# Kernel tuning notes

Hardware: AMD Instinct MI355X
Metric: run time of the kernel (lower is better)

Reference implementation:

```python
import jax, jax.numpy as jnp
import numpy as np

HID = 256
N, D, K, EPOCHS = 100000, 512, 5, 2


def _lin(x, w, b):
    return x @ w.T + b


def setup_inputs() -> dict:
    key = jax.random.key(0)
    ks = jax.random.split(key, 16)
    s = 0.05
    return {
        "x0": jax.random.normal(ks[0], (N, D), jnp.float32),
        "x1": jax.random.normal(ks[1], (N, D), jnp.float32),
        "Hin0_w": jax.random.normal(ks[2], (HID, D), jnp.float32) * s,
        "Hin0_b": jax.random.normal(ks[3], (HID,), jnp.float32) * s,
        "Hin1_w": jax.random.normal(ks[4], (HID, D), jnp.float32) * s,
        "Hin1_b": jax.random.normal(ks[5], (HID,), jnp.float32) * s,
        "w0_w": jax.random.normal(ks[6], (HID, HID), jnp.float32) * s,
        "w0_b": jax.random.normal(ks[7], (HID,), jnp.float32) * s,
        "w1_w": jax.random.normal(ks[8], (HID, HID), jnp.float32) * s,
        "w1_b": jax.random.normal(ks[9], (HID,), jnp.float32) * s,
        "w2_w": jax.random.normal(ks[10], (HID, HID), jnp.float32) * s,
        "w2_b": jax.random.normal(ks[11], (HID,), jnp.float32) * s,
        "edge0": jax.random.randint(ks[12], (2, N * K), 0, N, dtype=jnp.int32),
        "edge1": jax.random.randint(ks[13], (2, N * K), 0, N, dtype=jnp.int32),
        "k": K,
        "update_epoch": EPOCHS,
    }


def reference(x0, x1, Hin0_w, Hin0_b, Hin1_w, Hin1_b, w0_w, w0_b,
              w1_w, w1_b, w2_w, w2_b, edge0, edge1, k, update_epoch):
    xs = (x0, x1)
    edges = (edge0, edge1)
    Hws = ((Hin0_w, Hin0_b), (Hin1_w, Hin1_b))
    n_views = len(xs)

    # per-view input projections: h_init[v] = H_ins[v](train_view[v])
    h_inits = [_lin(x, w, b) for x, (w, b) in zip(xs, Hws)]

    finals = []
    for v in range(n_views):
        # neighbor table: node i's k neighbors are edge[1][i*k : (i+1)*k]
        nbr_idx = edges[v][1].reshape(-1, k)  # [N, k]
        # cross-view self term: mean over other views of w2(h_init_other)
        slf = _lin(h_inits[1 - v], w2_w, w2_b)  # [N, HID] (nv-1 == 1)
        h = h_inits[v]
        for _ in range(update_epoch):
            h = _lin(h, w0_w, w0_b)
            # mean_j w1(h[nbr_j]) == w1(mean_j h[nbr_j]) since w1 is affine
            nbr_mean = h[nbr_idx].mean(axis=1)  # [N, HID] gather + reduce
            h = h + _lin(nbr_mean, w1_w, w1_b) + slf
        finals.append(jax.nn.relu(h))

    # average final embeddings across views
    h_out = sum(finals) / n_views
    return h_out
```

## Files before the change

### kernel.cpp

```cpp
#include <hip/hip_runtime.h>

#define NN 100000
#define DD 512
#define HH 256
#define KNB 5

typedef __attribute__((ext_vector_type(8))) short short8v;
typedef __attribute__((ext_vector_type(4))) short short4v;
typedef __attribute__((ext_vector_type(4))) float float4v;

static __device__ __forceinline__ float bf2f(unsigned short u) {
  union { unsigned int i; float f; } c;
  c.i = ((unsigned int)u) << 16;
  return c.f;
}
static __device__ __forceinline__ unsigned short f2bf(float f) {
  union { float f; unsigned int i; } c;
  c.f = f;
  unsigned int u = c.i;
  u += 0x7FFFu + ((u >> 16) & 1u);
  return (unsigned short)(u >> 16);
}

#define GLOAD16(g, l) __builtin_amdgcn_global_load_lds( \
    (const __attribute__((address_space(1))) unsigned int*)(g), \
    (__attribute__((address_space(3))) unsigned int*)(l), 16, 0, 0)

__global__ void cvt2(const float* __restrict__ s0, short* __restrict__ d0,
                     const float* __restrict__ s1, short* __restrict__ d1) {
  const int S1 = (HH * DD) / 4;
  int i = blockIdx.x * blockDim.x + threadIdx.x;
  if (i >= 2 * S1) return;
  const float* s = (i < S1) ? s0 : s1;
  short* d = (i < S1) ? d0 : d1;
  int j = (i < S1) ? i : i - S1;
  float4 v = reinterpret_cast<const float4*>(s)[j];
  short4v o;
  o[0] = (short)f2bf(v.x); o[1] = (short)f2bf(v.y);
  o[2] = (short)f2bf(v.z); o[3] = (short)f2bf(v.w);
  reinterpret_cast<short4v*>(d)[j] = o;
}

__global__ void prep_w01(const float* __restrict__ w0, const float* __restrict__ w1,
                         const float* __restrict__ w2, const float* __restrict__ b0,
                         const float* __restrict__ b1, const float* __restrict__ b2,
                         short* __restrict__ Bcat, float* __restrict__ bc) {
  int i = blockIdx.x;
  int j = threadIdx.x;
  Bcat[(size_t)i * 768 + j]       = (short)f2bf(w0[i * 256 + j]);
  Bcat[(size_t)i * 768 + 512 + j] = (short)f2bf(w2[i * 256 + j]);
  float acc = 0.f;
  for (int k = 0; k < 256; ++k)
    acc = fmaf(w1[i * 256 + k], w0[k * 256 + j], acc);
  Bcat[(size_t)i * 768 + 256 + j] = (short)f2bf(acc);
  if (j == 0) {
    float s = b0[i] + b1[i] + b2[i];
    for (int k = 0; k < 256; ++k) s = fmaf(w1[i * 256 + k], b0[k], s);
    bc[i] = s;
  }
}

__global__ __launch_bounds__(512, 2) void proj_k(
    const float* __restrict__ Af0, const float* __restrict__ Af1,
    const short* __restrict__ Bw0, const short* __restrict__ Bw1,
    const float* __restrict__ bi0, const float* __restrict__ bi1,
    short* __restrict__ Cb0, short* __restrict__ Cb1)
{
  const float* Af = blockIdx.y ? Af1 : Af0;
  const short* Bw = blockIdx.y ? Bw1 : Bw0;
  const float* bias = blockIdx.y ? bi1 : bi0;
  short* Cb = blockIdx.y ? Cb1 : Cb0;

  __shared__ __align__(16) char BsRaw[2 * 256 * 64 * 2];
  __shared__ __align__(16) char AsRaw[2 * 64 * 64 * 2];

  const int tid = threadIdx.x;
  const int lane = tid & 63;
  const int wave = tid >> 6;
  const int wr = wave >> 2;
  const int wc = wave & 3;
  const int row0 = blockIdx.x * 64;

  const int sr = tid >> 3;
  const int slc = (tid & 7) ^ (sr & 7);
  const int srg = min(row0 + sr, NN - 1);
  const float* Asrc = Af + (size_t)srg * DD + slc * 8;

  int brow[4], blc[4];
#pragma unroll
  for (int q = 0; q < 4; ++q) {
    int ch = q * 512 + tid;
    brow[q] = ch >> 3;
    blc[q] = (ch & 7) ^ (brow[q] & 7);
  }

  float4v acc[2][4];
#pragma unroll
  for (int m = 0; m < 2; ++m)
#pragma unroll
    for (int n = 0; n < 4; ++n) acc[m][n] = (float4v)0.f;

  float4 pa[2][2];
  short8v pb[4];

#pragma unroll
  for (int q = 0; q < 4; ++q)
    pb[q] = *reinterpret_cast<const short8v*>(Bw + (size_t)brow[q] * DD + blc[q] * 8);
  {
    float4 f0 = *reinterpret_cast<const float4*>(Asrc);
    float4 f1 = *reinterpret_cast<const float4*>(Asrc + 4);
    short8v o;
    o[0] = (short)f2bf(f0.x); o[1] = (short)f2bf(f0.y);
    o[2] = (short)f2bf(f0.z); o[3] = (short)f2bf(f0.w);
    o[4] = (short)f2bf(f1.x); o[5] = (short)f2bf(f1.y);
    o[6] = (short)f2bf(f1.z); o[7] = (short)f2bf(f1.w);
    *reinterpret_cast<short8v*>(AsRaw + tid * 16) = o;
  }
#pragma unroll
  for (int q = 0; q < 4; ++q)
    *reinterpret_cast<short8v*>(BsRaw + (q * 512 + tid) * 16) = pb[q];
  pa[1][0] = *reinterpret_cast<const float4*>(Asrc + 64);
  pa[1][1] = *reinterpret_cast<const float4*>(Asrc + 68);
  __syncthreads();

#pragma unroll
  for (int s = 0; s < 8; ++s) {
    if (s + 1 < 8) {
#pragma unroll
      for (int q = 0; q < 4; ++q)
        pb[q] = *reinterpret_cast<const short8v*>(
            Bw + (size_t)brow[q] * DD + (s + 1) * 64 + blc[q] * 8);
    }
    if (s + 2 < 8) {
      pa[s & 1][0] = *reinterpret_cast<const float4*>(Asrc + (s + 2) * 64);
      pa[s & 1][1] = *reinterpret_cast<const float4*>(Asrc + (s + 2) * 64 + 4);
    }
    {
      const char* Bc = BsRaw + (s & 1) * 32768;
      const char* Ac = AsRaw + (s & 1) * 8192;
#pragma unroll
      for (int kk = 0; kk < 2; ++kk) {
        const int ckb = kk * 4 + (lane >> 4);
        short8v a[2], b[4];
#pragma unroll
        for (int n = 0; n < 4; ++n) {
          int rb = wc * 64 + n * 16 + (lane & 15);
          b[n] = *reinterpret_cast<const short8v*>(Bc + rb * 128 + ((ckb ^ (rb & 7)) << 4));
        }
#pragma unroll
        for (int m = 0; m < 2; ++m) {
          int ra = wr * 32 + m * 16 + (lane & 15);
          a[m] = *reinterpret_cast<const short8v*>(Ac + ra * 128 + ((ckb ^ (ra & 7)) << 4));
        }
#pragma unroll
        for (int m = 0; m < 2; ++m)
#pragma unroll
          for (int n = 0; n < 4; ++n)
            acc[m][n] = __builtin_amdgcn_mfma_f32_16x16x32_bf16(b[n], a[m], acc[m][n], 0, 0, 0);
      }
    }
    if (s + 1 < 8) {
      char* Bn = BsRaw + ((s + 1) & 1) * 32768;
#pragma unroll
      for (int q = 0; q < 4; ++q)
        *reinterpret_cast<short8v*>(Bn + (q * 512 + tid) * 16) = pb[q];
      float4 f0 = pa[(s + 1) & 1][0];
      float4 f1 = pa[(s + 1) & 1][1];
      short8v o;
      o[0] = (short)f2bf(f0.x); o[1] = (short)f2bf(f0.y);
      o[2] = (short)f2bf(f0.z); o[3] = (short)f2bf(f0.w);
      o[4] = (short)f2bf(f1.x); o[5] = (short)f2bf(f1.y);
      o[6] = (short)f2bf(f1.z); o[7] = (short)f2bf(f1.w);
      *reinterpret_cast<short8v*>(AsRaw + ((s + 1) & 1) * 8192 + tid * 16) = o;
    }
    __syncthreads();
  }

  const int crow = lane & 15;
  const int cg = (lane >> 4) * 4;
#pragma unroll
  for (int m = 0; m < 2; ++m) {
    int rg = row0 + wr * 32 + m * 16 + crow;
    if (rg >= NN) continue;
#pragma unroll
    for (int n = 0; n < 4; ++n) {
      int colb = wc * 64 + n * 16 + cg;
      size_t off = (size_t)rg * HH + colb;
      float4v bi = *reinterpret_cast<const float4v*>(bias + colb);
      short4v o;
#pragma unroll
      for (int i = 0; i < 4; ++i) o[i] = (short)f2bf(acc[m][n][i] + bi[i]);
      *reinterpret_cast<short4v*>(Cb + off) = o;
    }
  }
}

template<int EPI>
__global__ __launch_bounds__(512, 4) void epoch_k(
    const short* __restrict__ D, const short* __restrict__ Cc,
    const short* __restrict__ Bw, const float* __restrict__ bias,
    short* __restrict__ Ob, float* __restrict__ Of,
    const short* __restrict__ Fin, const int* __restrict__ nbr)
{
  __shared__ __align__(16) char BsRaw[256 * 64 * 2];
  __shared__ __align__(16) char AsRaw[128 * 64 * 2];
  __shared__ int nbrL[128][KNB];

  const int tid = threadIdx.x;
  const int lane = tid & 63;
  const int wave = tid >> 6;
  const int wr = wave >> 2;
  const int wc = wave & 3;
  const int row0 = blockIdx.x * 128;

  for (int e = tid; e < 128 * KNB; e += 512) {
    int r = e / KNB;
    int rg = min(row0 + r, NN - 1);
    nbrL[r][e - r * KNB] = nbr[rg * KNB + (e - r * KNB)];
  }

  float4v acc[4][4];
#pragma unroll
  for (int m = 0; m < 4; ++m)
#pragma unroll
    for (int n = 0; n < 4; ++n) acc[m][n] = (float4v)0.f;

  for (int k0 = 0; k0 < 768; k0 += 64) {
#pragma unroll
    for (int q = 0; q < 4; ++q) {
      int ch = q * 512 + tid;
      int r = ch >> 3, pc = ch & 7;
      int lc = pc ^ (r & 7);
      GLOAD16(Bw + (size_t)r * 768 + k0 + lc * 8, BsRaw + (q * 512 + wave * 64) * 16);
    }
    if (k0 < 256 || k0 >= 512) {
      const short* H = (k0 < 256) ? (D + k0) : (Cc + (k0 - 512));
#pragma unroll
      for (int q = 0; q < 2; ++q) {
        int ch = q * 512 + tid;
        int r = ch >> 3, pc = ch & 7;
        int lc = pc ^ (r & 7);
        int rg = min(row0 + r, NN - 1);
        GLOAD16(H + (size_t)rg * HH + lc * 8, AsRaw + (q * 512 + wave * 64) * 16);
      }
    } else {
      const int kb = k0 - 256;
#pragma unroll
      for (int q = 0; q < 2; ++q) {
        int ch = q * 512 + tid;
        int r = ch >> 3, pc = ch & 7;
        int lc = pc ^ (r & 7);
        float a8[8] = {0.f, 0.f, 0.f, 0.f, 0.f, 0.f, 0.f, 0.f};
#pragma unroll
        for (int j = 0; j < KNB; ++j) {
          int id = nbrL[r][j];
          short8v v = *reinterpret_cast<const short8v*>(D + (size_t)id * HH + kb + lc * 8);
#pragma unroll
          for (int x = 0; x < 8; ++x) a8[x] += bf2f((unsigned short)v[x]);
        }
        short8v o;
#pragma unroll
        for (int x = 0; x < 8; ++x) o[x] = (short)f2bf(a8[x] * 0.2f);
        *reinterpret_cast<short8v*>(AsRaw + ch * 16) = o;
      }
    }
    __syncthreads();

#pragma unroll
    for (int kk = 0; kk < 2; ++kk) {
      const int ckb = kk * 4 + (lane >> 4);
      short8v a[4], b[4];
#pragma unroll
      for (int n = 0; n < 4; ++n) {
        int rb = wc * 64 + n * 16 + (lane & 15);
        b[n] = *reinterpret_cast<const short8v*>(BsRaw + rb * 128 + ((ckb ^ (rb & 7)) << 4));
      }
#pragma unroll
      for (int m = 0; m < 4; ++m) {
        int ra = wr * 64 + m * 16 + (lane & 15);
        a[m] = *reinterpret_cast<const short8v*>(AsRaw + ra * 128 + ((ckb ^ (ra & 7)) << 4));
      }
#pragma unroll
      for (int m = 0; m < 4; ++m)
#pragma unroll
        for (int n = 0; n < 4; ++n)
          acc[m][n] = __builtin_amdgcn_mfma_f32_16x16x32_bf16(b[n], a[m], acc[m][n], 0, 0, 0);
    }
    __syncthreads();
  }

  const int crow = lane & 15;
  const int cg = (lane >> 4) * 4;
#pragma unroll
  for (int m = 0; m < 4; ++m) {
    int rg = row0 + wr * 64 + m * 16 + crow;
    if (rg >= NN) continue;
#pragma unroll
    for (int n = 0; n < 4; ++n) {
      int colb = wc * 64 + n * 16 + cg;
      size_t off = (size_t)rg * HH + colb;
      float4v bi = *reinterpret_cast<const float4v*>(bias + colb);
      float v[4];
#pragma unroll
      for (int i = 0; i < 4; ++i) v[i] = acc[m][n][i] + bi[i];
      if constexpr (EPI >= 2) {
#pragma unroll
        for (int i = 0; i < 4; ++i) v[i] = fmaxf(v[i], 0.f);
      }
      if constexpr (EPI <= 2) {
        short4v o;
#pragma unroll
        for (int i = 0; i < 4; ++i) o[i] = (short)f2bf(v[i]);
        *reinterpret_cast<short4v*>(Ob + off) = o;
      } else {
        short4v f4 = *reinterpret_cast<const short4v*>(Fin + off);
        float4v o;
#pragma unroll
        for (int i = 0; i < 4; ++i)
          o[i] = (v[i] + bf2f((unsigned short)f4[i])) * 0.5f;
        *reinterpret_cast<float4v*>(Of + off) = o;
      }
    }
  }
}

extern "C" void kernel_launch(void* const* d_in, const int* in_sizes, int n_in,
                              void* d_out, int out_size, void* d_ws, size_t ws_size,
                              hipStream_t stream) {
  const float* x0  = (const float*)d_in[0];
  const float* x1  = (const float*)d_in[1];
  const float* wh0 = (const float*)d_in[2];
  const float* bh0 = (const float*)d_in[3];
  const float* wh1 = (const float*)d_in[4];
  const float* bh1 = (const float*)d_in[5];
  const float* w0  = (const float*)d_in[6];
  const float* b0  = (const float*)d_in[7];
  const float* w1  = (const float*)d_in[8];
  const float* b1  = (const float*)d_in[9];
  const float* w2  = (const float*)d_in[10];
  const float* b2  = (const float*)d_in[11];
  const int* e0    = (const int*)d_in[12];
  const int* e1    = (const int*)d_in[13];
  const int* nbr0  = e0 + (size_t)NN * KNB;
  const int* nbr1  = e1 + (size_t)NN * KNB;
  float* out       = (float*)d_out;

  char* ws = (char*)d_ws;
  size_t off = 0;
  auto alloc = [&](size_t bytes) -> void* {
    off = (off + 255) & ~(size_t)255;
    void* p = ws + off;
    off += bytes;
    return p;
  };

  short* Wh0  = (short*)alloc((size_t)HH * DD * 2);
  short* Wh1  = (short*)alloc((size_t)HH * DD * 2);
  short* Bcat = (short*)alloc((size_t)HH * 768 * 2);
  float* bc   = (float*)alloc((size_t)HH * 4);
  const size_t NB = (size_t)NN * HH * 2;
  short* hi0 = (short*)alloc(NB);
  short* hi1 = (short*)alloc(NB);
  short* hb0 = (short*)alloc(NB);
  short* hb1 = (short*)alloc(NB);
  short* f0  = (short*)alloc(NB);

  cvt2<<<dim3(256), dim3(256), 0, stream>>>(wh0, Wh0, wh1, Wh1);
  prep_w01<<<dim3(256), dim3(256), 0, stream>>>(w0, w1, w2, b0, b1, b2, Bcat, bc);

  proj_k<<<dim3((NN + 63) / 64, 2), dim3(512), 0, stream>>>(
      x0, x1, Wh0, Wh1, bh0, bh1, hi0, hi1);

  dim3 ge((NN + 127) / 128);

  epoch_k<0><<<ge, dim3(512), 0, stream>>>(hi0, hi1, Bcat, bc, hb0, nullptr, nullptr, nbr0);
  epoch_k<0><<<ge, dim3(512), 0, stream>>>(hi1, hi0, Bcat, bc, hb1, nullptr, nullptr, nbr1);

  epoch_k<2><<<ge, dim3(512), 0, stream>>>(hb0, hi1, Bcat, bc, f0, nullptr, nullptr, nbr0);
  epoch_k<3><<<ge, dim3(512), 0, stream>>>(hb1, hi0, Bcat, bc, nullptr, out, f0, nbr1);

  (void)in_sizes; (void)n_in; (void)out_size; (void)ws_size;
}
```

Measured before the change: 532.6 us.

## Double-buffer epoch GEMM stages and merge first-epoch views into one launch

Rewrites the epoch kernel's K loop as an explicitly unrolled, double-buffered pipeline. The next stage's async global-to-LDS loads are issued while the current stage's MFMAs run, using manual vmcnt waits and raw barriers in place of __syncthreads. The two first-epoch launches are merged into one launch with a 2D grid that picks the view from blockIdx.y. The aim is to hide load latency and cut launch overhead and tail effects, at the cost of doubled LDS use (about 96KB), which lowers occupancy, and the launch-bounds occupancy hint is dropped.

```diff
diff --git a/kernel.cpp b/kernel.cpp
--- a/kernel.cpp
+++ b/kernel.cpp
@@ -25,6 +25,10 @@
 #define GLOAD16(g, l) __builtin_amdgcn_global_load_lds( \
     (const __attribute__((address_space(1))) unsigned int*)(g), \
     (__attribute__((address_space(3))) unsigned int*)(l), 16, 0, 0)
+
+#define WAITV(N) asm volatile("s_waitcnt vmcnt(" #N ")" ::: "memory")
+#define WAITL()  asm volatile("s_waitcnt lgkmcnt(0)" ::: "memory")
+#define BAR()    __builtin_amdgcn_s_barrier()
 
 __global__ void cvt2(const float* __restrict__ s0, short* __restrict__ d0,
                      const float* __restrict__ s1, short* __restrict__ d1) {
@@ -196,15 +200,22 @@
 }
 
 template<int EPI>
-__global__ __launch_bounds__(512, 4) void epoch_k(
-    const short* __restrict__ D, const short* __restrict__ Cc,
+__global__ __launch_bounds__(512) void epoch_p(
+    const short* __restrict__ D0_, const short* __restrict__ C0_,
+    short* __restrict__ O0_, const int* __restrict__ n0_,
+    const short* __restrict__ D1_, const short* __restrict__ C1_,
+    short* __restrict__ O1_, const int* __restrict__ n1_,
     const short* __restrict__ Bw, const float* __restrict__ bias,
-    short* __restrict__ Ob, float* __restrict__ Of,
-    const short* __restrict__ Fin, const int* __restrict__ nbr)
+    float* __restrict__ Of, const short* __restrict__ Fin)
 {
-  __shared__ __align__(16) char BsRaw[256 * 64 * 2];
-  __shared__ __align__(16) char AsRaw[128 * 64 * 2];
+  __shared__ __align__(16) char BsRaw[2 * 256 * 64 * 2];
+  __shared__ __align__(16) char AsRaw[2 * 128 * 64 * 2];
   __shared__ int nbrL[128][KNB];
+
+  const short* D  = blockIdx.y ? D1_ : D0_;
+  const short* Cc = blockIdx.y ? C1_ : C0_;
+  short* Ob       = blockIdx.y ? O1_ : O0_;
+  const int* nbr  = blockIdx.y ? n1_ : n0_;
 
   const int tid = threadIdx.x;
   const int lane = tid & 63;
@@ -213,81 +224,104 @@
   const int wc = wave & 3;
   const int row0 = blockIdx.x * 128;
 
+  float4v acc[4][4];
+#pragma unroll
+  for (int m = 0; m < 4; ++m)
+#pragma unroll
+    for (int n = 0; n < 4; ++n) acc[m][n] = (float4v)0.f;
+
+  auto issue_dense = [&](int sn, const short* Ps) {
+    char* Bn = BsRaw + (sn & 1) * 32768;
+    char* An = AsRaw + (sn & 1) * 16384;
+#pragma unroll
+    for (int q = 0; q < 4; ++q) {
+      int ch = q * 512 + tid;
+      int r = ch >> 3, lc = (ch & 7) ^ ((ch >> 3) & 7);
+      GLOAD16(Bw + (size_t)r * 768 + sn * 64 + lc * 8, Bn + (q * 512 + wave * 64) * 16);
+    }
+#pragma unroll
+    for (int q = 0; q < 2; ++q) {
+      int ch = q * 512 + tid;
+      int r = ch >> 3, lc = (ch & 7) ^ ((ch >> 3) & 7);
+      int rg = min(row0 + r, NN - 1);
+      GLOAD16(Ps + (size_t)rg * HH + lc * 8, An + (q * 512 + wave * 64) * 16);
+    }
+  };
+  auto issue_B = [&](int sn) {
+    char* Bn = BsRaw + (sn & 1) * 32768;
+#pragma unroll
+    for (int q = 0; q < 4; ++q) {
+      int ch = q * 512 + tid;
+      int r = ch >> 3, lc = (ch & 7) ^ ((ch >> 3) & 7);
+      GLOAD16(Bw + (size_t)r * 768 + sn * 64 + lc * 8, Bn + (q * 512 + wave * 64) * 16);
+    }
+  };
+  auto gather_A = [&](int sn) {
+    char* An = AsRaw + (sn & 1) * 16384;
+    const int kb = sn * 64 - 256;
+#pragma unroll
+    for (int q = 0; q < 2; ++q) {
+      int ch = q * 512 + tid;
+      int r = ch >> 3, lc = (ch & 7) ^ ((ch >> 3) & 7);
+      float a8[8] = {0.f, 0.f, 0.f, 0.f, 0.f, 0.f, 0.f, 0.f};
+#pragma unroll
+      for (int j = 0; j < KNB; ++j) {
+        int id = nbrL[r][j];
+        short8v v = *reinterpret_cast<const short8v*>(D + (size_t)id * HH + kb + lc * 8);
+#pragma unroll
+        for (int x = 0; x < 8; ++x) a8[x] += bf2f((unsigned short)v[x]);
+      }
+      short8v o;
+#pragma unroll
+      for (int x = 0; x < 8; ++x) o[x] = (short)f2bf(a8[x] * 0.2f);
+      *reinterpret_cast<short8v*>(An + ch * 16) = o;
+    }
+  };
+  auto compute = [&](int s) {
+    const char* Bc = BsRaw + (s & 1) * 32768;
+    const char* Ac = AsRaw + (s & 1) * 16384;
+#pragma unroll
+    for (int kk = 0; kk < 2; ++kk) {
+      const int ckb = kk * 4 + (lane >> 4);
+      short8v a[4], b[4];
+#pragma unroll
+      for (int n = 0; n < 4; ++n) {
+        int rb = wc * 64 + n * 16 + (lane & 15);
+        b[n] = *reinterpret_cast<const short8v*>(Bc + rb * 128 + ((ckb ^ (rb & 7)) << 4));
+      }
+#pragma unroll
+      for (int m = 0; m < 4; ++m) {
+        int ra = wr * 64 + m * 16 + (lane & 15);
+        a[m] = *reinterpret_cast<const short8v*>(Ac + ra * 128 + ((ckb ^ (ra & 7)) << 4));
+      }
+#pragma unroll
+      for (int m = 0; m < 4; ++m)
+#pragma unroll
+        for (int n = 0; n < 4; ++n)
+          acc[m][n] = __builtin_amdgcn_mfma_f32_16x16x32_bf16(b[n], a[m], acc[m][n], 0, 0, 0);
+    }
+  };
+
   for (int e = tid; e < 128 * KNB; e += 512) {
     int r = e / KNB;
     int rg = min(row0 + r, NN - 1);
     nbrL[r][e - r * KNB] = nbr[rg * KNB + (e - r * KNB)];
   }
-
-  float4v acc[4][4];
-#pragma unroll
-  for (int m = 0; m < 4; ++m)
-#pragma unroll
-    for (int n = 0; n < 4; ++n) acc[m][n] = (float4v)0.f;
-
-  for (int k0 = 0; k0 < 768; k0 += 64) {
-#pragma unroll
-    for (int q = 0; q < 4; ++q) {
-      int ch = q * 512 + tid;
-      int r = ch >> 3, pc = ch & 7;
-      int lc = pc ^ (r & 7);
-      GLOAD16(Bw + (size_t)r * 768 + k0 + lc * 8, BsRaw + (q * 512 + wave * 64) * 16);
-    }
-    if (k0 < 256 || k0 >= 512) {
-      const short* H = (k0 < 256) ? (D + k0) : (Cc + (k0 - 512));
-#pragma unroll
-      for (int q = 0; q < 2; ++q) {
-        int ch = q * 512 + tid;
-        int r = ch >> 3, pc = ch & 7;
-        int lc = pc ^ (r & 7);
-        int rg = min(row0 + r, NN - 1);
-        GLOAD16(H + (size_t)rg * HH + lc * 8, AsRaw + (q * 512 + wave * 64) * 16);
-      }
-    } else {
-      const int kb = k0 - 256;
-#pragma unroll
-      for (int q = 0; q < 2; ++q) {
-        int ch = q * 512 + tid;
-        int r = ch >> 3, pc = ch & 7;
-        int lc = pc ^ (r & 7);
-        float a8[8] = {0.f, 0.f, 0.f, 0.f, 0.f, 0.f, 0.f, 0.f};
-#pragma unroll
-        for (int j = 0; j < KNB; ++j) {
-          int id = nbrL[r][j];
-          short8v v = *reinterpret_cast<const short8v*>(D + (size_t)id * HH + kb + lc * 8);
-#pragma unroll
-          for (int x = 0; x < 8; ++x) a8[x] += bf2f((unsigned short)v[x]);
-        }
-        short8v o;
-#pragma unroll
-        for (int x = 0; x < 8; ++x) o[x] = (short)f2bf(a8[x] * 0.2f);
-        *reinterpret_cast<short8v*>(AsRaw + ch * 16) = o;
-      }
-    }
-    __syncthreads();
-
-#pragma unroll
-    for (int kk = 0; kk < 2; ++kk) {
-      const int ckb = kk * 4 + (lane >> 4);
-      short8v a[4], b[4];
-#pragma unroll
-      for (int n = 0; n < 4; ++n) {
-        int rb = wc * 64 + n * 16 + (lane & 15);
-        b[n] = *reinterpret_cast<const short8v*>(BsRaw + rb * 128 + ((ckb ^ (rb & 7)) << 4));
-      }
-#pragma unroll
-      for (int m = 0; m < 4; ++m) {
-        int ra = wr * 64 + m * 16 + (lane & 15);
-        a[m] = *reinterpret_cast<const short8v*>(AsRaw + ra * 128 + ((ckb ^ (ra & 7)) << 4));
-      }
-#pragma unroll
-      for (int m = 0; m < 4; ++m)
-#pragma unroll
-        for (int n = 0; n < 4; ++n)
-          acc[m][n] = __builtin_amdgcn_mfma_f32_16x16x32_bf16(b[n], a[m], acc[m][n], 0, 0, 0);
-    }
-    __syncthreads();
-  }
+  issue_dense(0, D);
+  WAITL();
+
+  issue_dense(1, D + 64);   WAITV(6); BAR(); compute(0);  BAR();
+  issue_dense(2, D + 128);  WAITV(6); BAR(); compute(1);  BAR();
+  issue_dense(3, D + 192);  WAITV(6); BAR(); compute(2);  BAR();
+  issue_B(4);  WAITV(4); BAR(); compute(3);  gather_A(4); WAITL(); BAR();
+  issue_B(5);  WAITV(4); BAR(); compute(4);  gather_A(5); WAITL(); BAR();
+  issue_B(6);  WAITV(4); BAR(); compute(5);  gather_A(6); WAITL(); BAR();
+  issue_B(7);  WAITV(4); BAR(); compute(6);  gather_A(7); WAITL(); BAR();
+  issue_dense(8, Cc);       WAITV(6); BAR(); compute(7);  BAR();
+  issue_dense(9, Cc + 64);  WAITV(6); BAR(); compute(8);  BAR();
+  issue_dense(10, Cc + 128); WAITV(6); BAR(); compute(9);  BAR();
+  issue_dense(11, Cc + 192); WAITV(6); BAR(); compute(10); BAR();
+  WAITV(0); BAR(); compute(11);
 
   const int crow = lane & 15;
   const int cg = (lane >> 4) * 4;
@@ -373,11 +407,14 @@
 
   dim3 ge((NN + 127) / 128);
 
-  epoch_k<0><<<ge, dim3(512), 0, stream>>>(hi0, hi1, Bcat, bc, hb0, nullptr, nullptr, nbr0);
-  epoch_k<0><<<ge, dim3(512), 0, stream>>>(hi1, hi0, Bcat, bc, hb1, nullptr, nullptr, nbr1);
-
-  epoch_k<2><<<ge, dim3(512), 0, stream>>>(hb0, hi1, Bcat, bc, f0, nullptr, nullptr, nbr0);
-  epoch_k<3><<<ge, dim3(512), 0, stream>>>(hb1, hi0, Bcat, bc, nullptr, out, f0, nbr1);
+  epoch_p<0><<<dim3(ge.x, 2), dim3(512), 0, stream>>>(
+      hi0, hi1, hb0, nbr0,  hi1, hi0, hb1, nbr1,  Bcat, bc, nullptr, nullptr);
+
+  epoch_p<2><<<dim3(ge.x, 1), dim3(512), 0, stream>>>(
+      hb0, hi1, f0, nbr0,   hb0, hi1, f0, nbr0,   Bcat, bc, nullptr, nullptr);
+
+  epoch_p<3><<<dim3(ge.x, 1), dim3(512), 0, stream>>>(
+      hb1, hi0, nullptr, nbr1,  hb1, hi0, nullptr, nbr1,  Bcat, bc, out, f0);
 
   (void)in_sizes; (void)n_in; (void)out_size; (void)ws_size;
 }
```

Result: slower. 556.3 us (+4.4%).
